# Kernel optimization log

Hardware: AMD Instinct MI355X
Metric: run time of the kernel (lower is better)

Reference implementation:

```python
import math
import jax, jax.numpy as jnp
import numpy as np

B, N, C = 64, 197, 768
H = 12
D = C // H
SCALE = D ** -0.5
EPS_SM = 1e-6
LN_EPS = 1e-5


def _layernorm(x, w, b):
    mu = jnp.mean(x, axis=-1, keepdims=True)
    var = jnp.var(x, axis=-1, keepdims=True)
    return (x - mu) * jax.lax.rsqrt(var + LN_EPS) * w + b


def setup_inputs() -> dict:
    key = jax.random.key(0)
    ks = jax.random.split(key, 12)
    s = 0.02
    return {
        "x": jax.random.normal(ks[0], (B, N, C), jnp.float32),
        "mask": jnp.ones((B, N), jnp.float32),
        "ln1_w": jnp.ones((C,), jnp.float32),
        "ln1_b": jnp.zeros((C,), jnp.float32),
        "qkv_w": jax.random.normal(ks[1], (C, 3 * C), jnp.float32) * s,
        "qkv_b": jnp.zeros((3 * C,), jnp.float32),
        "proj_w": jax.random.normal(ks[2], (C, C), jnp.float32) * s,
        "proj_b": jnp.zeros((C,), jnp.float32),
        "ln2_w": jnp.ones((C,), jnp.float32),
        "ln2_b": jnp.zeros((C,), jnp.float32),
        "fc1_w": jax.random.normal(ks[3], (C, 4 * C), jnp.float32) * s,
        "fc1_b": jnp.zeros((4 * C,), jnp.float32),
        "fc2_w": jax.random.normal(ks[4], (4 * C, C), jnp.float32) * s,
        "fc2_b": jnp.zeros((C,), jnp.float32),
        "threshold": jnp.float32(0.0),
    }


def reference(x, mask, ln1_w, ln1_b, qkv_w, qkv_b, proj_w, proj_b,
              ln2_w, ln2_b, fc1_w, fc1_b, fc2_w, fc2_b, threshold):
    # --- LTPAttention ---
    h = _layernorm(x, ln1_w, ln1_b)
    qkv = (h @ qkv_w + qkv_b).reshape(B, N, 3, H, D)
    qkv = jnp.transpose(qkv, (2, 0, 3, 1, 4))  # (3, B, H, N, D)
    q, k, v = qkv[0], qkv[1], qkv[2]
    attn = jnp.einsum("bhnd,bhmd->bhnm", q, k) * SCALE  # (B,H,N,N)
    # softmax_with_mask (eval path): exp * key-mask, renormalize
    m = mask[:, None, None, :]  # (B,1,1,N) masks keys
    w = jnp.exp(attn - jnp.max(attn, axis=-1, keepdims=True)) * m
    attn = w / (jnp.sum(w, axis=-1, keepdims=True) + EPS_SM)
    out = jnp.einsum("bhnm,bhmd->bhnd", attn, v)
    out = jnp.transpose(out, (0, 2, 1, 3)).reshape(B, N, C)
    x_attn = out @ proj_w + proj_b
    # importance scores: mean over heads and queries -> (B, N)
    imp = jnp.mean(attn, axis=(1, 2))
    imp = imp.at[:, 0].set(jnp.inf)  # always keep CLS token
    # ThresholdMasker (eval): hard threshold
    new_mask = (imp > threshold).astype(mask.dtype)
    mask_out = jnp.where(mask > 0, new_mask, mask)
    # --- residual + MLP ---
    x = x + x_attn
    h2 = _layernorm(x, ln2_w, ln2_b)
    h2 = jax.nn.gelu(h2 @ fc1_w + fc1_b, approximate=False)
    x = x + (h2 @ fc2_w + fc2_b)
    return x, mask_out
```

## Files before the change

### kernel.cpp

```cpp
#include <hip/hip_runtime.h>
#include <hip/hip_bf16.h>
#include <math.h>

#define B_ 64
#define N_ 197
#define C_ 768
#define H_ 12
#define BN_ (B_ * N_)
#define GRIDM64 197

typedef unsigned short ushort_t;
typedef __attribute__((ext_vector_type(8))) short short8;
typedef __attribute__((ext_vector_type(4))) float f32x4;

__device__ __forceinline__ float wave_reduce_sum(float v) {
#pragma unroll
  for (int off = 32; off; off >>= 1) v += __shfl_xor(v, off);
  return v;
}

__device__ __forceinline__ ushort_t f2bf(float f) {
  __hip_bfloat16 h = __float2bfloat16(f);
  ushort_t u;
  __builtin_memcpy(&u, &h, 2);
  return u;
}

__device__ __forceinline__ float gelu_fast(float u) {
  const float z2 = 1.5957691216f * (u + 0.044715f * u * u * u);
  const float e = __expf(z2);
  const float th = 1.f - 2.f / (e + 1.f);
  return 0.5f * u * (1.f + th);
}

__global__ __launch_bounds__(256) void wtrans_kernel(const float* __restrict__ W,
                                                     ushort_t* __restrict__ Wt,
                                                     int K, int N) {
  __shared__ ushort_t tile[32][33];
  const int bn = blockIdx.x * 32, bk = blockIdx.y * 32;
  const int tx = threadIdx.x & 31, ty = threadIdx.x >> 5;
#pragma unroll
  for (int i = ty; i < 32; i += 8)
    tile[i][tx] = f2bf(W[(size_t)(bk + i) * N + bn + tx]);
  __syncthreads();
#pragma unroll
  for (int i = ty; i < 32; i += 8)
    Wt[(size_t)(bn + i) * K + bk + tx] = tile[tx][i];
}

__global__ __launch_bounds__(256) void ln_kernel(const float* __restrict__ x,
                                                 const float* __restrict__ w,
                                                 const float* __restrict__ bsh,
                                                 ushort_t* __restrict__ out) {
  const int row = blockIdx.x;
  const float* xr = x + (size_t)row * C_;
  const int tid = threadIdx.x;
  float v0 = xr[tid], v1 = xr[tid + 256], v2 = xr[tid + 512];
  float s = v0 + v1 + v2;
  float q = v0 * v0 + v1 * v1 + v2 * v2;
  s = wave_reduce_sum(s);
  q = wave_reduce_sum(q);
  __shared__ float red[8];
  const int w4 = tid >> 6, l = tid & 63;
  if (l == 0) { red[w4] = s; red[4 + w4] = q; }
  __syncthreads();
  float ts = red[0] + red[1] + red[2] + red[3];
  float tq = red[4] + red[5] + red[6] + red[7];
  float mu = ts * (1.f / C_);
  float var = tq * (1.f / C_) - mu * mu;
  float rs = rsqrtf(var + 1e-5f);
  ushort_t* orow = out + (size_t)row * C_;
  orow[tid]       = f2bf((v0 - mu) * rs * w[tid]       + bsh[tid]);
  orow[tid + 256] = f2bf((v1 - mu) * rs * w[tid + 256] + bsh[tid + 256]);
  orow[tid + 512] = f2bf((v2 - mu) * rs * w[tid + 512] + bsh[tid + 512]);
}

template <int RES, int ACT, int OUT_BF16>
__global__ __launch_bounds__(64) void mfma_gemm(const ushort_t* __restrict__ A,
                                                const ushort_t* __restrict__ Bt,
                                                const float* __restrict__ bias,
                                                const float* __restrict__ res,
                                                void* __restrict__ Cout,
                                                int M, int Nc, int K, int gridN) {
  __shared__ __align__(16) ushort_t As0[64][32];
  __shared__ __align__(16) ushort_t As1[64][32];
  __shared__ __align__(16) ushort_t Bs0[64][32];
  __shared__ __align__(16) ushort_t Bs1[64][32];

  const int flat = blockIdx.x;
  const int x8 = flat & 7, q8 = flat >> 3;
  const int n_t = q8 % gridN, jj = q8 / gridN;
  const int m_t = jj * 8 + x8;
  if (m_t >= GRIDM64) return;

  const int l = threadIdx.x;
  const int quad = l >> 4, lm = l & 15;
  const int bm = m_t * 64, bnn = n_t * 64;

  const int srow = l >> 2;
  const int scol = ((l & 3) ^ ((l >> 3) & 3)) << 3;
  const ushort_t* ap[4];
  const ushort_t* bp[4];
#pragma unroll
  for (int i = 0; i < 4; i++) {
    ap[i] = A + (size_t)(bm + i * 16 + srow) * K + scol;
    bp[i] = Bt + (size_t)(bnn + i * 16 + srow) * K + scol;
  }

  auto stage = [&](ushort_t (*Ad)[32], ushort_t (*Bd)[32]) {
#pragma unroll
    for (int i = 0; i < 4; i++) {
      __builtin_amdgcn_global_load_lds(
          (const __attribute__((address_space(1))) void*)ap[i],
          (__attribute__((address_space(3))) void*)&Ad[i * 16][0], 16, 0, 0);
      ap[i] += 32;
    }
#pragma unroll
    for (int i = 0; i < 4; i++) {
      __builtin_amdgcn_global_load_lds(
          (const __attribute__((address_space(1))) void*)bp[i],
          (__attribute__((address_space(3))) void*)&Bd[i * 16][0], 16, 0, 0);
      bp[i] += 32;
    }
  };

  const int fslot = (quad ^ ((lm >> 1) & 3)) << 3;

  f32x4 acc[4][4];
#pragma unroll
  for (int mi = 0; mi < 4; mi++)
#pragma unroll
    for (int ni = 0; ni < 4; ni++) acc[mi][ni] = (f32x4){0.f, 0.f, 0.f, 0.f};

  const int NIT = K >> 5;

#define GSTEP(Ac, Bc, An, Bn, VMN, DOSTAGE)                              \
  {                                                                      \
    if (DOSTAGE) stage(An, Bn);                                          \
    asm volatile("s_waitcnt vmcnt(" #VMN ")" ::: "memory");              \
    __builtin_amdgcn_sched_barrier(0);                                   \
    short8 af[4], bf[4];                                                 \
    _Pragma("unroll") for (int i = 0; i < 4; i++) {                      \
      af[i] = *(const short8*)&Ac[i * 16 + lm][fslot];                   \
      bf[i] = *(const short8*)&Bc[i * 16 + lm][fslot];                   \
    }                                                                    \
    _Pragma("unroll") for (int mi = 0; mi < 4; mi++)                     \
      _Pragma("unroll") for (int ni = 0; ni < 4; ni++)                   \
        acc[mi][ni] = __builtin_amdgcn_mfma_f32_16x16x32_bf16(           \
            af[mi], bf[ni], acc[mi][ni], 0, 0, 0);                       \
  }

  stage(As0, Bs0);
  int t = 0;
  for (; t + 2 < NIT; t += 2) {
    GSTEP(As0, Bs0, As1, Bs1, 8, 1);
    GSTEP(As1, Bs1, As0, Bs0, 8, 1);
  }
  GSTEP(As0, Bs0, As1, Bs1, 8, 1);
  GSTEP(As1, Bs1, As0, Bs0, 0, 0);
#undef GSTEP

#pragma unroll
  for (int mi = 0; mi < 4; mi++) {
#pragma unroll
    for (int ni = 0; ni < 4; ni++) {
      const int col = bnn + ni * 16 + lm;
      const float bv = bias[col];
#pragma unroll
      for (int r = 0; r < 4; r++) {
        const int row = bm + mi * 16 + quad * 4 + r;
        float v = acc[mi][ni][r] + bv;
        if constexpr (RES) v += res[(size_t)row * Nc + col];
        if constexpr (ACT) v = gelu_fast(v);
        if constexpr (OUT_BF16)
          ((ushort_t*)Cout)[(size_t)row * Nc + col] = f2bf(v);
        else
          ((float*)Cout)[(size_t)row * Nc + col] = v;
      }
    }
  }
}

__global__ __launch_bounds__(256, 2) void attn_mfma(const ushort_t* __restrict__ qkv,
                                                    const float* __restrict__ mask,
                                                    ushort_t* __restrict__ aout,
                                                    float* __restrict__ imp) {
  __shared__ __align__(16) ushort_t Ks[208 * 64];
  __shared__ __align__(16) ushort_t Vt[64 * 216];
  __shared__ __align__(16) ushort_t Pb[4][16 * 208];
  const int b = blockIdx.x / H_, h = blockIdx.x % H_;
  const int tid = threadIdx.x, w = tid >> 6, l = tid & 63;
  const int quad = l >> 4, lm = l & 15;
  const ushort_t* qbase = qkv + (size_t)b * N_ * 2304 + h * 64;
  const ushort_t* kbase = qbase + 768;
  const ushort_t* vbase = qbase + 1536;

  for (int idx = tid; idx < 208 * 8; idx += 256) {
    const int j = idx >> 3, g = idx & 7;
    uint4 val = make_uint4(0u, 0u, 0u, 0u);
    if (j < N_) val = *(const uint4*)(kbase + (size_t)j * 2304 + g * 8);
    *(uint4*)&Ks[j * 64 + ((g ^ (j & 7)) << 3)] = val;
  }
  for (int idx = tid; idx < 52 * 64; idx += 256) {
    const int d = idx & 63, jg = idx >> 6, j0 = jg * 4;
    ushort_t a0 = 0, a1 = 0, a2 = 0, a3 = 0;
    if (j0 + 0 < N_) a0 = vbase[(size_t)(j0 + 0) * 2304 + d];
    if (j0 + 1 < N_) a1 = vbase[(size_t)(j0 + 1) * 2304 + d];
    if (j0 + 2 < N_) a2 = vbase[(size_t)(j0 + 2) * 2304 + d];
    if (j0 + 3 < N_) a3 = vbase[(size_t)(j0 + 3) * 2304 + d];
    uint2 pk;
    pk.x = (unsigned)a0 | ((unsigned)a1 << 16);
    pk.y = (unsigned)a2 | ((unsigned)a3 << 16);
    *(uint2*)&Vt[d * 216 + j0] = pk;
  }
  float mkv[13];
#pragma unroll
  for (int t = 0; t < 13; t++) {
    const int col = t * 16 + lm;
    mkv[t] = (col < N_) ? mask[b * N_ + col] : 0.f;
  }
  float cs[13];
#pragma unroll
  for (int t = 0; t < 13; t++) cs[t] = 0.f;
  __syncthreads();

  ushort_t* pw = &Pb[w][0];
  for (int i0 = w * 16; i0 < 208; i0 += 64) {
    f32x4 accs[13];
#pragma unroll
    for (int t = 0; t < 13; t++) accs[t] = (f32x4){0.f, 0.f, 0.f, 0.f};
#pragma unroll
    for (int kh = 0; kh < 2; kh++) {
      const int k0 = kh * 32;
      const short8 aq =
          *(const short8*)(qbase + (size_t)(i0 + lm) * 2304 + k0 + quad * 8);
      const int gb = (k0 >> 3) + quad;
#pragma unroll
      for (int t = 0; t < 13; t++) {
        const int j = t * 16 + lm;
        const short8 bk = *(const short8*)&Ks[j * 64 + ((gb ^ (j & 7)) << 3)];
        accs[t] = __builtin_amdgcn_mfma_f32_16x16x32_bf16(aq, bk, accs[t], 0, 0, 0);
      }
    }
    float inv[4];
#pragma unroll
    for (int r = 0; r < 4; r++) {
      float m = -3.4e38f;
#pragma unroll
      for (int t = 0; t < 13; t++) m = fmaxf(m, accs[t][r] * 0.125f);
      m = fmaxf(m, __shfl_xor(m, 1));
      m = fmaxf(m, __shfl_xor(m, 2));
      m = fmaxf(m, __shfl_xor(m, 4));
      m = fmaxf(m, __shfl_xor(m, 8));
      float s = 0.f;
#pragma unroll
      for (int t = 0; t < 13; t++) {
        const float e = __expf(accs[t][r] * 0.125f - m) * mkv[t];
        accs[t][r] = e;
        s += e;
      }
      s += __shfl_xor(s, 1);
      s += __shfl_xor(s, 2);
      s += __shfl_xor(s, 4);
      s += __shfl_xor(s, 8);
      inv[r] = 1.f / (s + 1e-6f);
    }
    const int ibase = i0 + quad * 4;
#pragma unroll
    for (int r = 0; r < 4; r++) {
      const bool rok = (ibase + r) < N_;
#pragma unroll
      for (int t = 0; t < 13; t++) {
        const float p = accs[t][r] * inv[r];
        accs[t][r] = p;
        if (rok) cs[t] += p;
        pw[(quad * 4 + r) * 208 + t * 16 + lm] = f2bf(p);
      }
    }
    __builtin_amdgcn_wave_barrier();
    f32x4 acco[4];
#pragma unroll
    for (int n = 0; n < 4; n++) acco[n] = (f32x4){0.f, 0.f, 0.f, 0.f};
#pragma unroll
    for (int ks = 0; ks < 6; ks++) {
      const int k0 = ks * 32;
      const short8 ap = *(const short8*)&pw[lm * 208 + k0 + quad * 8];
#pragma unroll
      for (int n = 0; n < 4; n++) {
        const short8 bv = *(const short8*)&Vt[(n * 16 + lm) * 216 + k0 + quad * 8];
        acco[n] = __builtin_amdgcn_mfma_f32_16x16x32_bf16(ap, bv, acco[n], 0, 0, 0);
      }
    }
    {
      const bool lo = (quad < 2);
      short8 apt = {};
      if (lo) apt = *(const short8*)&pw[lm * 208 + 192 + quad * 8];
#pragma unroll
      for (int n = 0; n < 4; n++) {
        short8 bvt = {};
        if (lo) bvt = *(const short8*)&Vt[(n * 16 + lm) * 216 + 192 + quad * 8];
        acco[n] = __builtin_amdgcn_mfma_f32_16x16x32_bf16(apt, bvt, acco[n], 0, 0, 0);
      }
    }
#pragma unroll
    for (int r = 0; r < 4; r++) {
      const int i = ibase + r;
      if (i < N_) {
#pragma unroll
        for (int n = 0; n < 4; n++)
          aout[(size_t)(b * N_ + i) * C_ + h * 64 + n * 16 + lm] = f2bf(acco[n][r]);
      }
    }
  }
#pragma unroll
  for (int t = 0; t < 13; t++) {
    float v = cs[t];
    v += __shfl_xor(v, 16);
    v += __shfl_xor(v, 32);
    if (l < 16) {
      const int col = t * 16 + l;
      if (col < N_)
        atomicAdd(&imp[b * N_ + col], v * (1.f / (H_ * (float)N_)));
    }
  }
}

__global__ __launch_bounds__(256) void mask_kernel(const float* __restrict__ imp,
                                                   const float* __restrict__ mask,
                                                   const float* __restrict__ thr,
                                                   float* __restrict__ mask_out) {
  const int i = blockIdx.x * 256 + threadIdx.x;
  if (i >= BN_) return;
  const int n = i % N_;
  const float iv = (n == 0) ? INFINITY : imp[i];
  const float m = mask[i];
  const float nm = (iv > thr[0]) ? 1.f : 0.f;
  mask_out[i] = (m > 0.f) ? nm : m;
}

extern "C" void kernel_launch(void* const* d_in, const int* in_sizes, int n_in,
                              void* d_out, int out_size, void* d_ws, size_t ws_size,
                              hipStream_t stream) {
  const float* x      = (const float*)d_in[0];
  const float* mask   = (const float*)d_in[1];
  const float* ln1_w  = (const float*)d_in[2];
  const float* ln1_b  = (const float*)d_in[3];
  const float* qkv_w  = (const float*)d_in[4];
  const float* qkv_b  = (const float*)d_in[5];
  const float* proj_w = (const float*)d_in[6];
  const float* proj_b = (const float*)d_in[7];
  const float* ln2_w  = (const float*)d_in[8];
  const float* ln2_b  = (const float*)d_in[9];
  const float* fc1_w  = (const float*)d_in[10];
  const float* fc1_b  = (const float*)d_in[11];
  const float* fc2_w  = (const float*)d_in[12];
  const float* fc2_b  = (const float*)d_in[13];
  const float* thr    = (const float*)d_in[14];

  float* out = (float*)d_out;
  float* mask_out = out + (size_t)BN_ * C_;

  ushort_t* buf0    = (ushort_t*)d_ws;
  ushort_t* hbuf    = buf0 + (size_t)BN_ * 3072;
  ushort_t* aoutb   = hbuf + (size_t)BN_ * 768;
  ushort_t* qkv_wt  = aoutb + (size_t)BN_ * 768;
  ushort_t* proj_wt = qkv_wt + (size_t)2304 * 768;
  ushort_t* fc1_wt  = proj_wt + (size_t)768 * 768;
  ushort_t* fc2_wt  = fc1_wt + (size_t)3072 * 768;
  float*    impb    = (float*)(fc2_wt + (size_t)768 * 3072);

  hipMemsetAsync(impb, 0, BN_ * sizeof(float), stream);

  wtrans_kernel<<<dim3(2304 / 32, 768 / 32), 256, 0, stream>>>(qkv_w, qkv_wt, 768, 2304);
  wtrans_kernel<<<dim3(768 / 32, 768 / 32), 256, 0, stream>>>(proj_w, proj_wt, 768, 768);
  wtrans_kernel<<<dim3(3072 / 32, 768 / 32), 256, 0, stream>>>(fc1_w, fc1_wt, 768, 3072);
  wtrans_kernel<<<dim3(768 / 32, 3072 / 32), 256, 0, stream>>>(fc2_w, fc2_wt, 3072, 768);

  const int MS = 25 * 8;
  ln_kernel<<<BN_, 256, 0, stream>>>(x, ln1_w, ln1_b, hbuf);
  mfma_gemm<0, 0, 1><<<MS * 36, 64, 0, stream>>>(
      hbuf, qkv_wt, qkv_b, nullptr, buf0, BN_, 2304, 768, 36);
  attn_mfma<<<B_ * H_, 256, 0, stream>>>(buf0, mask, aoutb, impb);
  mask_kernel<<<(BN_ + 255) / 256, 256, 0, stream>>>(impb, mask, thr, mask_out);
  mfma_gemm<1, 0, 0><<<MS * 12, 64, 0, stream>>>(
      aoutb, proj_wt, proj_b, x, out, BN_, 768, 768, 12);
  ln_kernel<<<BN_, 256, 0, stream>>>(out, ln2_w, ln2_b, hbuf);
  mfma_gemm<0, 1, 1><<<MS * 48, 64, 0, stream>>>(
      hbuf, fc1_wt, fc1_b, nullptr, buf0, BN_, 3072, 768, 48);
  mfma_gemm<1, 0, 0><<<MS * 12, 64, 0, stream>>>(
      buf0, fc2_wt, fc2_b, out, out, BN_, 768, 3072, 12);
}
```

Baseline: 651.8 us.

## Load GEMM MFMA fragments directly from global memory, dropping LDS staging

Replaces the double-buffered global_load_lds staging with direct per-lane 16-byte global loads of A and B fragments straight into registers for each MFMA step. This removes LDS usage, the swizzle logic and the explicit vmcnt waits, and the loop is left to a compiler unroll of 2. In exchange it loses explicit prefetch overlap and relies on L1/L2 to serve the repeated row reads. The global accesses are also strided rows with only 64 bytes contiguous per row per step, which may stall the MFMAs on memory latency.

```diff
diff --git a/kernel.cpp b/kernel.cpp
--- a/kernel.cpp
+++ b/kernel.cpp
@@ -82,11 +82,6 @@
                                                 const float* __restrict__ res,
                                                 void* __restrict__ Cout,
                                                 int M, int Nc, int K, int gridN) {
-  __shared__ __align__(16) ushort_t As0[64][32];
-  __shared__ __align__(16) ushort_t As1[64][32];
-  __shared__ __align__(16) ushort_t Bs0[64][32];
-  __shared__ __align__(16) ushort_t Bs1[64][32];
-
   const int flat = blockIdx.x;
   const int x8 = flat & 7, q8 = flat >> 3;
   const int n_t = q8 % gridN, jj = q8 / gridN;
@@ -97,68 +92,33 @@
   const int quad = l >> 4, lm = l & 15;
   const int bm = m_t * 64, bnn = n_t * 64;
 
-  const int srow = l >> 2;
-  const int scol = ((l & 3) ^ ((l >> 3) & 3)) << 3;
-  const ushort_t* ap[4];
-  const ushort_t* bp[4];
-#pragma unroll
-  for (int i = 0; i < 4; i++) {
-    ap[i] = A + (size_t)(bm + i * 16 + srow) * K + scol;
-    bp[i] = Bt + (size_t)(bnn + i * 16 + srow) * K + scol;
-  }
-
-  auto stage = [&](ushort_t (*Ad)[32], ushort_t (*Bd)[32]) {
+  const ushort_t* arow0 = A + (size_t)(bm + lm) * K + quad * 8;
+  const ushort_t* brow0 = Bt + (size_t)(bnn + lm) * K + quad * 8;
+  const size_t rstep = (size_t)16 * K;
+
+  f32x4 acc[4][4];
+#pragma unroll
+  for (int mi = 0; mi < 4; mi++)
+#pragma unroll
+    for (int ni = 0; ni < 4; ni++) acc[mi][ni] = (f32x4){0.f, 0.f, 0.f, 0.f};
+
+  const int NIT = K >> 5;
+#pragma unroll 2
+  for (int t = 0; t < NIT; ++t) {
+    const int ko = t * 32;
+    short8 af[4], bf[4];
 #pragma unroll
     for (int i = 0; i < 4; i++) {
-      __builtin_amdgcn_global_load_lds(
-          (const __attribute__((address_space(1))) void*)ap[i],
-          (__attribute__((address_space(3))) void*)&Ad[i * 16][0], 16, 0, 0);
-      ap[i] += 32;
-    }
-#pragma unroll
-    for (int i = 0; i < 4; i++) {
-      __builtin_amdgcn_global_load_lds(
-          (const __attribute__((address_space(1))) void*)bp[i],
-          (__attribute__((address_space(3))) void*)&Bd[i * 16][0], 16, 0, 0);
-      bp[i] += 32;
-    }
-  };
-
-  const int fslot = (quad ^ ((lm >> 1) & 3)) << 3;
-
-  f32x4 acc[4][4];
-#pragma unroll
-  for (int mi = 0; mi < 4; mi++)
-#pragma unroll
-    for (int ni = 0; ni < 4; ni++) acc[mi][ni] = (f32x4){0.f, 0.f, 0.f, 0.f};
-
-  const int NIT = K >> 5;
-
-#define GSTEP(Ac, Bc, An, Bn, VMN, DOSTAGE)                              \
-  {                                                                      \
-    if (DOSTAGE) stage(An, Bn);                                          \
-    asm volatile("s_waitcnt vmcnt(" #VMN ")" ::: "memory");              \
-    __builtin_amdgcn_sched_barrier(0);                                   \
-    short8 af[4], bf[4];                                                 \
-    _Pragma("unroll") for (int i = 0; i < 4; i++) {                      \
-      af[i] = *(const short8*)&Ac[i * 16 + lm][fslot];                   \
-      bf[i] = *(const short8*)&Bc[i * 16 + lm][fslot];                   \
-    }                                                                    \
-    _Pragma("unroll") for (int mi = 0; mi < 4; mi++)                     \
-      _Pragma("unroll") for (int ni = 0; ni < 4; ni++)                   \
-        acc[mi][ni] = __builtin_amdgcn_mfma_f32_16x16x32_bf16(           \
-            af[mi], bf[ni], acc[mi][ni], 0, 0, 0);                       \
-  }
-
-  stage(As0, Bs0);
-  int t = 0;
-  for (; t + 2 < NIT; t += 2) {
-    GSTEP(As0, Bs0, As1, Bs1, 8, 1);
-    GSTEP(As1, Bs1, As0, Bs0, 8, 1);
-  }
-  GSTEP(As0, Bs0, As1, Bs1, 8, 1);
-  GSTEP(As1, Bs1, As0, Bs0, 0, 0);
-#undef GSTEP
+      af[i] = *(const short8*)(arow0 + (size_t)i * rstep + ko);
+      bf[i] = *(const short8*)(brow0 + (size_t)i * rstep + ko);
+    }
+#pragma unroll
+    for (int mi = 0; mi < 4; mi++)
+#pragma unroll
+      for (int ni = 0; ni < 4; ni++)
+        acc[mi][ni] = __builtin_amdgcn_mfma_f32_16x16x32_bf16(af[mi], bf[ni],
+                                                              acc[mi][ni], 0, 0, 0);
+  }
 
 #pragma unroll
   for (int mi = 0; mi < 4; mi++) {
```

Result: slower. 935.4 us (+43.5%).
